# Optimization experiments

Hardware: AMD Instinct MI355X
Metric: run time of the kernel (lower is better)

## Reference

```python
import jax, jax.numpy as jnp
import numpy as np

B, N, D, H = 2, 1024, 1024, 16
DH = D // H
SCALE = 1.0 / DH ** 0.5
STJ_Q = 1.0
NUM_ITER = 4
CAUSAL = True
EPS = 1e-6


def setup_inputs() -> dict:
    key = jax.random.key(0)
    k1, k2, k3 = jax.random.split(key, 3)
    x = jax.random.normal(k1, (B, N, D), jnp.float32)
    Wqkv = jax.random.normal(k2, (3 * D, D), jnp.float32) / np.float32(np.sqrt(D))
    Wo = jax.random.normal(k3, (D, D), jnp.float32) / np.float32(np.sqrt(D))
    return {"x": x, "Wqkv": Wqkv, "Wo": Wo}


def stieltjes_attention(Q, K, V, scale, causal, q, num_iter):
    # Q,K,V: [B,H,N,dh]. Scores s: [B,H,N,N].
    n = Q.shape[2]
    s = jnp.einsum('bhnd,bhmd->bhnm', Q, K) * scale
    if causal:
        mask = jnp.tril(jnp.ones((n, n), bool))  # [N,N], True = attend
    else:
        mask = jnp.ones((n, n), bool)
    # Solve per-row lambda s.t. sum_j (lambda - s_j)^(-q) = 1 (Stieltjes-transform
    # normalization) with Newton iterations; masked entries contribute 0.
    s_masked = jnp.where(mask, s, -1e30)
    lam = s_masked.max(-1) + 1.0  # [B,H,N], start above max score
    for _ in range(num_iter):
        d = jnp.maximum(lam[..., None] - s, EPS)  # [B,H,N,N]
        w = jnp.where(mask, d ** (-q), 0.0)
        f = w.sum(-1) - 1.0
        fp = -q * jnp.where(mask, d ** (-q - 1.0), 0.0).sum(-1)
        lam = lam - f / fp
    d = jnp.maximum(lam[..., None] - s, EPS)
    p = jnp.where(mask, d ** (-q), 0.0)
    p = p / p.sum(-1, keepdims=True)  # final exact normalization
    return jnp.einsum('bhnm,bhmd->bhnd', p, V)


def reference(x, Wqkv, Wo):
    b, n, dmodel = x.shape
    qkv = (x @ Wqkv.T).reshape(b, n, 3, H, DH).transpose(2, 0, 3, 1, 4)
    Q, K, V = qkv[0], qkv[1], qkv[2]
    o = stieltjes_attention(Q, K, V, SCALE, CAUSAL, STJ_Q, NUM_ITER)
    o = o.transpose(0, 2, 1, 3).reshape(b, n, dmodel)
    return o @ Wo.T
```

## Files before the change

kernel.cpp:

```cpp
#include <hip/hip_runtime.h>
#include <hip/hip_bf16.h>
#include <math.h>

#define HNUM 16
#define DH 64
#define NSEQ 1024
#define BATCH 2
#define DMODEL 1024
#define SCALE 0.125f
#define EPS 1e-6f
#define NUM_ITER 4
#define SPAD 1128

typedef float f32x4 __attribute__((ext_vector_type(4)));
typedef short bfrag __attribute__((ext_vector_type(8)));
typedef unsigned int u32x4 __attribute__((ext_vector_type(4)));

__device__ inline float bf2f_u(unsigned int u) {
    return __builtin_bit_cast(float, u << 16);
}
__device__ inline unsigned short f2bf_u(float f) {
    return __builtin_bit_cast(unsigned short, __float2bfloat16(f));
}

__device__ inline void gload16(const __hip_bfloat16* g, __hip_bfloat16* l) {
    __builtin_amdgcn_global_load_lds(
        (const __attribute__((address_space(1))) void*)g,
        (__attribute__((address_space(3))) void*)l, 16, 0, 0);
}

__global__ __launch_bounds__(256) void cast3(const float* __restrict__ s0, __hip_bfloat16* __restrict__ d0, int n0,
                                             const float* __restrict__ s1, __hip_bfloat16* __restrict__ d1, int n1,
                                             const float* __restrict__ s2, __hip_bfloat16* __restrict__ d2, int n2) {
    const int stride = gridDim.x * blockDim.x;
    const int tot = n0 + n1 + n2;
    for (int i = blockIdx.x * blockDim.x + threadIdx.x; i < tot; i += stride) {
        const float* s; __hip_bfloat16* d; int off;
        if (i < n0)            { s = s0; d = d0; off = i; }
        else if (i < n0 + n1)  { s = s1; d = d1; off = i - n0; }
        else                   { s = s2; d = d2; off = i - n0 - n1; }
        const float4 v = *reinterpret_cast<const float4*>(&s[(size_t)off * 4]);
        ushort4 o;
        o.x = f2bf_u(v.x); o.y = f2bf_u(v.y); o.z = f2bf_u(v.z); o.w = f2bf_u(v.w);
        *reinterpret_cast<ushort4*>(&d[(size_t)off * 4]) = o;
    }
}

template <bool OUT_BF16>
__global__ __launch_bounds__(256) void gemm_bt(const __hip_bfloat16* __restrict__ A,
                                               const __hip_bfloat16* __restrict__ B,
                                               void* __restrict__ Cv,
                                               int M, int Nc, int K) {
    __shared__ __align__(16) __hip_bfloat16 As[128 * 64];
    __shared__ __align__(16) __hip_bfloat16 Bs[128 * 64];
    const int tid  = threadIdx.x;
    const int l    = tid & 63;
    const int wave = tid >> 6;
    const int m0 = blockIdx.y * 128, n0 = blockIdx.x * 128;
    const int wr = (wave >> 1) * 64, wc = (wave & 1) * 64;
    const int lr = l & 15;
    const int lk = (l >> 4) * 8;

    f32x4 acc[4][4];
#pragma unroll
    for (int m = 0; m < 4; ++m)
#pragma unroll
        for (int n = 0; n < 4; ++n) acc[m][n] = (f32x4){0.f, 0.f, 0.f, 0.f};

    for (int k0 = 0; k0 < K; k0 += 64) {
#pragma unroll
        for (int p = 0; p < 4; ++p) {
            const int idx = tid + p * 256;
            const int r = idx >> 3, ce = (idx & 7) * 8;
            gload16(&A[(size_t)(m0 + r) * K + k0 + ce], &As[idx * 8]);
        }
#pragma unroll
        for (int p = 0; p < 4; ++p) {
            const int idx = tid + p * 256;
            const int r = idx >> 3, ce = (idx & 7) * 8;
            gload16(&B[(size_t)(n0 + r) * K + k0 + ce], &Bs[idx * 8]);
        }
        __syncthreads();

#pragma unroll
        for (int kk = 0; kk < 64; kk += 32) {
            bfrag af[4], bfr[4];
#pragma unroll
            for (int m = 0; m < 4; ++m)
                af[m] = *reinterpret_cast<const bfrag*>(&As[(wr + m * 16 + lr) * 64 + kk + lk]);
#pragma unroll
            for (int n = 0; n < 4; ++n)
                bfr[n] = *reinterpret_cast<const bfrag*>(&Bs[(wc + n * 16 + lr) * 64 + kk + lk]);
#pragma unroll
            for (int m = 0; m < 4; ++m)
#pragma unroll
                for (int n = 0; n < 4; ++n)
                    acc[m][n] = __builtin_amdgcn_mfma_f32_16x16x32_bf16(
                        af[m], bfr[n], acc[m][n], 0, 0, 0);
        }
        __syncthreads();
    }

#pragma unroll
    for (int m = 0; m < 4; ++m) {
        const int row0 = m0 + wr + m * 16 + (l >> 4) * 4;
#pragma unroll
        for (int n = 0; n < 4; ++n) {
            const int col = n0 + wc + n * 16 + lr;
#pragma unroll
            for (int j = 0; j < 4; ++j) {
                if constexpr (OUT_BF16) {
                    ((__hip_bfloat16*)Cv)[(size_t)(row0 + j) * Nc + col] =
                        __float2bfloat16(acc[m][n][j]);
                } else {
                    ((float*)Cv)[(size_t)(row0 + j) * Nc + col] = acc[m][n][j];
                }
            }
        }
    }
}

__global__ __launch_bounds__(256) void transpose_v(const __hip_bfloat16* __restrict__ qkvb,
                                                   __hip_bfloat16* __restrict__ Vt) {
    const int bh = blockIdx.x >> 4;
    const int nc = blockIdx.x & 15;
    const int b = bh >> 4, h = bh & 15;
    __shared__ unsigned short tile[64][80];
    const int t = threadIdx.x;
    {
        const int r = t >> 2, cc = (t & 3) * 16;
        const size_t src = ((size_t)(b * NSEQ + nc * 64 + r)) * 3072 + 2048 + h * 64 + cc;
        const uint4 v0 = *reinterpret_cast<const uint4*>(&qkvb[src]);
        const uint4 v1 = *reinterpret_cast<const uint4*>(&qkvb[src + 8]);
        *reinterpret_cast<uint4*>(&tile[r][cc])     = v0;
        *reinterpret_cast<uint4*>(&tile[r][cc + 8]) = v1;
    }
    __syncthreads();
    {
        const int d = t >> 2, n2 = (t & 3) * 16;
        unsigned int e[16];
#pragma unroll
        for (int k = 0; k < 16; ++k) e[k] = tile[n2 + k][d];
        uint4 o0, o1;
        o0.x = e[0]  | (e[1]  << 16); o0.y = e[2]  | (e[3]  << 16);
        o0.z = e[4]  | (e[5]  << 16); o0.w = e[6]  | (e[7]  << 16);
        o1.x = e[8]  | (e[9]  << 16); o1.y = e[10] | (e[11] << 16);
        o1.z = e[12] | (e[13] << 16); o1.w = e[14] | (e[15] << 16);
        const size_t dst = ((size_t)(bh * 64 + d)) * 1024 + nc * 64 + n2;
        *reinterpret_cast<uint4*>(&Vt[dst])     = o0;
        *reinterpret_cast<uint4*>(&Vt[dst + 8]) = o1;
    }
}

template <int NQ>
__device__ inline void newton_row_wb(unsigned short* __restrict__ Srow,
                                     int ncols, int limit, int lane) {
    constexpr int NC = NQ * 2;
    float sv[NC * 2];
#pragma unroll
    for (int t = 0; t < NC; ++t) {
        const int c = lane * 2 + t * 128;
        const unsigned int u = *reinterpret_cast<const unsigned int*>(&Srow[c]);
        float v0 = bf2f_u(u & 0xffffu);
        float v1 = bf2f_u(u >> 16);
        if (t >= NC - 2) {
            v0 = (c     < ncols) ? v0 : -1e30f;
            v1 = (c + 1 < ncols) ? v1 : -1e30f;
        }
        sv[2 * t] = v0; sv[2 * t + 1] = v1;
    }

    float mx = sv[0];
#pragma unroll
    for (int e = 1; e < 2 * NC; ++e) mx = fmaxf(mx, sv[e]);
#pragma unroll
    for (int off = 32; off; off >>= 1) mx = fmaxf(mx, __shfl_xor(mx, off));
    float lam = mx + 1.0f;

    for (int it = 0; it < NUM_ITER; ++it) {
        float f = 0.f, fp = 0.f;
#pragma unroll
        for (int e = 0; e < 2 * NC; ++e) {
            const float inv = __builtin_amdgcn_rcpf(fmaxf(lam - sv[e], EPS));
            f += inv; fp = fmaf(inv, inv, fp);
        }
#pragma unroll
        for (int off = 32; off; off >>= 1) {
            f  += __shfl_xor(f, off);
            fp += __shfl_xor(fp, off);
        }
        lam += (f - 1.0f) / fp;
    }

    float sw = 0.f;
#pragma unroll
    for (int e = 0; e < 2 * NC; ++e) {
        sv[e] = __builtin_amdgcn_rcpf(fmaxf(lam - sv[e], EPS));
        sw += sv[e];
    }
#pragma unroll
    for (int off = 32; off; off >>= 1) sw += __shfl_xor(sw, off);
    const float isw = __builtin_amdgcn_rcpf(sw);

#pragma unroll
    for (int t = 0; t < NC; ++t) {
        const int c = lane * 2 + t * 128;
        if (t * 128 < limit && c < limit) {
            const unsigned int pk = (unsigned)f2bf_u(sv[2 * t] * isw)
                                  | ((unsigned)f2bf_u(sv[2 * t + 1] * isw) << 16);
            *reinterpret_cast<unsigned int*>(&Srow[c]) = pk;
        }
    }
}

__global__ __launch_bounds__(512) void attn_mfma(const __hip_bfloat16* __restrict__ qkvb,
                                                 const __hip_bfloat16* __restrict__ Vt,
                                                 __hip_bfloat16* __restrict__ obf) {
    const int tid  = threadIdx.x;
    const int lane = tid & 63;
    const int wave = tid >> 6;
    const int qt = blockIdx.x & 63;
    const int bh = blockIdx.x >> 6;
    const int b = bh >> 4, h = bh & 15;
    const int r0 = qt * 16;

    __shared__ __align__(16) unsigned short S[16][SPAD];
    __shared__ __align__(16) unsigned short Qs[16][72];

    const size_t qbase = (size_t)(b * NSEQ) * 3072;
    const int lr  = lane & 15;
    const int lk8 = (lane >> 4) * 8;

    if (tid < 128) {
        const int r = tid >> 3, c = (tid & 7) * 8;
        const uint4 v = *reinterpret_cast<const uint4*>(
            &qkvb[qbase + (size_t)(r0 + r) * 3072 + h * 64 + c]);
        *reinterpret_cast<uint4*>(&Qs[r][c]) = v;
    }
    __syncthreads();

    const __hip_bfloat16* kglob = qkvb + qbase + 1024 + h * 64;
    const int ntask = qt + 1;
    const bfrag a0 = *reinterpret_cast<const bfrag*>(&Qs[lr][lk8]);
    const bfrag a1 = *reinterpret_cast<const bfrag*>(&Qs[lr][32 + lk8]);
    for (int jt = wave; jt < ntask; jt += 8) {
        const int jrow = jt * 16 + lr;
        const bfrag b0 = *reinterpret_cast<const bfrag*>(&kglob[(size_t)jrow * 3072 + lk8]);
        const bfrag b1 = *reinterpret_cast<const bfrag*>(&kglob[(size_t)jrow * 3072 + 32 + lk8]);
        f32x4 c = (f32x4){0.f, 0.f, 0.f, 0.f};
        c = __builtin_amdgcn_mfma_f32_16x16x32_bf16(a0, b0, c, 0, 0, 0);
        c = __builtin_amdgcn_mfma_f32_16x16x32_bf16(a1, b1, c, 0, 0, 0);
#pragma unroll
        for (int j = 0; j < 4; ++j) {
            const int row = (lane >> 4) * 4 + j;
            S[row][jt * 16 + lr] = f2bf_u(c[j] * SCALE);
        }
    }
    __syncthreads();

    if (tid < 192) {
        const int row = tid / 12;
        const int cu  = tid - row * 12;
        *reinterpret_cast<u32x4*>(&S[row][r0 + 16 + cu * 8]) = (u32x4){0u, 0u, 0u, 0u};
    }
    const int limit = r0 + 16;
    for (int rr = 0; rr < 2; ++rr) {
        const int row   = wave * 2 + rr;
        const int ncols = r0 + row + 1;
        const int nq    = (ncols + 255) >> 8;
        switch (nq) {
            case 1:  newton_row_wb<1>(S[row], ncols, limit, lane); break;
            case 2:  newton_row_wb<2>(S[row], ncols, limit, lane); break;
            case 3:  newton_row_wb<3>(S[row], ncols, limit, lane); break;
            default: newton_row_wb<4>(S[row], ncols, limit, lane); break;
        }
    }
    __syncthreads();

    if (wave < 4) {
        const int dt = wave;
        const __hip_bfloat16* vtrow = Vt + ((size_t)(bh * 64 + dt * 16 + lr)) * 1024;

        f32x4 acc0 = (f32x4){0.f, 0.f, 0.f, 0.f};
        f32x4 acc1 = (f32x4){0.f, 0.f, 0.f, 0.f};
        for (int j0 = 0; j0 <= r0; j0 += 64) {
            {
                const bfrag pa = *reinterpret_cast<const bfrag*>(&S[lr][j0 + lk8]);
                const bfrag pb = *reinterpret_cast<const bfrag*>(&vtrow[j0 + lk8]);
                acc0 = __builtin_amdgcn_mfma_f32_16x16x32_bf16(pa, pb, acc0, 0, 0, 0);
            }
            if (j0 + 32 <= r0) {
                const bfrag pa = *reinterpret_cast<const bfrag*>(&S[lr][j0 + 32 + lk8]);
                const bfrag pb = *reinterpret_cast<const bfrag*>(&vtrow[j0 + 32 + lk8]);
                acc1 = __builtin_amdgcn_mfma_f32_16x16x32_bf16(pa, pb, acc1, 0, 0, 0);
            }
        }

#pragma unroll
        for (int j = 0; j < 4; ++j) {
            const int row = (lane >> 4) * 4 + j;
            obf[(size_t)(b * NSEQ + r0 + row) * 1024 + h * 64 + dt * 16 + lr] =
                __float2bfloat16(acc0[j] + acc1[j]);
        }
    }
}

extern "C" void kernel_launch(void* const* d_in, const int* in_sizes, int n_in,
                              void* d_out, int out_size, void* d_ws, size_t ws_size,
                              hipStream_t stream) {
    const float* x    = (const float*)d_in[0];
    const float* Wqkv = (const float*)d_in[1];
    const float* Wo   = (const float*)d_in[2];
    float* out = (float*)d_out;

    const int M = BATCH * NSEQ;
    char* ws = (char*)d_ws;
    __hip_bfloat16* xbf  = (__hip_bfloat16*)ws; ws += (size_t)M * DMODEL * 2;
    __hip_bfloat16* wqbf = (__hip_bfloat16*)ws; ws += (size_t)3 * DMODEL * DMODEL * 2;
    __hip_bfloat16* wobf = (__hip_bfloat16*)ws; ws += (size_t)DMODEL * DMODEL * 2;
    __hip_bfloat16* qkvb = (__hip_bfloat16*)ws; ws += (size_t)M * 3 * DMODEL * 2;
    __hip_bfloat16* Vt   = (__hip_bfloat16*)ws; ws += (size_t)BATCH * HNUM * DH * NSEQ * 2;
    __hip_bfloat16* obf  = (__hip_bfloat16*)ws; ws += (size_t)M * DMODEL * 2;

    dim3 blk(256);
    cast3<<<2048, blk, 0, stream>>>(x, xbf, M * DMODEL / 4,
                                    Wqkv, wqbf, 3 * DMODEL * DMODEL / 4,
                                    Wo, wobf, DMODEL * DMODEL / 4);

    dim3 g1(3 * DMODEL / 128, M / 128);
    gemm_bt<true><<<g1, blk, 0, stream>>>(xbf, wqbf, qkvb, M, 3 * DMODEL, DMODEL);

    transpose_v<<<512, blk, 0, stream>>>(qkvb, Vt);

    attn_mfma<<<2048, dim3(512), 0, stream>>>(qkvb, Vt, obf);

    dim3 g2(DMODEL / 128, M / 128);
    gemm_bt<false><<<g2, blk, 0, stream>>>(obf, wobf, out, M, DMODEL, DMODEL);
}
```

Baseline: 125.2 us.

## Shrink GEMM M-tile, interleave two Newton rows per wave, load Q fragments directly

The GEMM tile shrinks from 128x128 to 64x128, which doubles the grid size so more workgroups are in flight on the many compute units, at the cost of less reuse of each B tile. The Newton solver now processes a wave's two rows together, so the two independent reductions and reciprocal chains can hide each other's latency. Q fragments are read straight from global memory instead of being staged in LDS, which removes the Qs buffer and one barrier. Zeroing of the padding tile is folded into the score loop, and the S row padding is reduced to cut LDS use.

```diff
diff --git a/kernel.cpp b/kernel.cpp
--- a/kernel.cpp
+++ b/kernel.cpp
@@ -10,7 +10,7 @@
 #define SCALE 0.125f
 #define EPS 1e-6f
 #define NUM_ITER 4
-#define SPAD 1128
+#define SPAD 1048
 
 typedef float f32x4 __attribute__((ext_vector_type(4)));
 typedef short bfrag __attribute__((ext_vector_type(8)));
@@ -51,25 +51,25 @@
                                                const __hip_bfloat16* __restrict__ B,
                                                void* __restrict__ Cv,
                                                int M, int Nc, int K) {
-    __shared__ __align__(16) __hip_bfloat16 As[128 * 64];
+    __shared__ __align__(16) __hip_bfloat16 As[64 * 64];
     __shared__ __align__(16) __hip_bfloat16 Bs[128 * 64];
     const int tid  = threadIdx.x;
     const int l    = tid & 63;
     const int wave = tid >> 6;
-    const int m0 = blockIdx.y * 128, n0 = blockIdx.x * 128;
-    const int wr = (wave >> 1) * 64, wc = (wave & 1) * 64;
+    const int m0 = blockIdx.y * 64, n0 = blockIdx.x * 128;
+    const int wr = (wave >> 1) * 32, wc = (wave & 1) * 64;
     const int lr = l & 15;
     const int lk = (l >> 4) * 8;
 
-    f32x4 acc[4][4];
-#pragma unroll
-    for (int m = 0; m < 4; ++m)
+    f32x4 acc[2][4];
+#pragma unroll
+    for (int m = 0; m < 2; ++m)
 #pragma unroll
         for (int n = 0; n < 4; ++n) acc[m][n] = (f32x4){0.f, 0.f, 0.f, 0.f};
 
     for (int k0 = 0; k0 < K; k0 += 64) {
 #pragma unroll
-        for (int p = 0; p < 4; ++p) {
+        for (int p = 0; p < 2; ++p) {
             const int idx = tid + p * 256;
             const int r = idx >> 3, ce = (idx & 7) * 8;
             gload16(&A[(size_t)(m0 + r) * K + k0 + ce], &As[idx * 8]);
@@ -84,15 +84,15 @@
 
 #pragma unroll
         for (int kk = 0; kk < 64; kk += 32) {
-            bfrag af[4], bfr[4];
-#pragma unroll
-            for (int m = 0; m < 4; ++m)
+            bfrag af[2], bfr[4];
+#pragma unroll
+            for (int m = 0; m < 2; ++m)
                 af[m] = *reinterpret_cast<const bfrag*>(&As[(wr + m * 16 + lr) * 64 + kk + lk]);
 #pragma unroll
             for (int n = 0; n < 4; ++n)
                 bfr[n] = *reinterpret_cast<const bfrag*>(&Bs[(wc + n * 16 + lr) * 64 + kk + lk]);
 #pragma unroll
-            for (int m = 0; m < 4; ++m)
+            for (int m = 0; m < 2; ++m)
 #pragma unroll
                 for (int n = 0; n < 4; ++n)
                     acc[m][n] = __builtin_amdgcn_mfma_f32_16x16x32_bf16(
@@ -102,7 +102,7 @@
     }
 
 #pragma unroll
-    for (int m = 0; m < 4; ++m) {
+    for (int m = 0; m < 2; ++m) {
         const int row0 = m0 + wr + m * 16 + (l >> 4) * 4;
 #pragma unroll
         for (int n = 0; n < 4; ++n) {
@@ -153,62 +153,80 @@
 }
 
 template <int NQ>
-__device__ inline void newton_row_wb(unsigned short* __restrict__ Srow,
-                                     int ncols, int limit, int lane) {
+__device__ inline void newton2_wb(unsigned short* __restrict__ SA,
+                                  unsigned short* __restrict__ SB,
+                                  int ncolsA, int ncolsB, int limit, int lane) {
     constexpr int NC = NQ * 2;
-    float sv[NC * 2];
+    float svA[NC * 2], svB[NC * 2];
 #pragma unroll
     for (int t = 0; t < NC; ++t) {
         const int c = lane * 2 + t * 128;
-        const unsigned int u = *reinterpret_cast<const unsigned int*>(&Srow[c]);
-        float v0 = bf2f_u(u & 0xffffu);
-        float v1 = bf2f_u(u >> 16);
+        const unsigned int uA = *reinterpret_cast<const unsigned int*>(&SA[c]);
+        const unsigned int uB = *reinterpret_cast<const unsigned int*>(&SB[c]);
+        float a0 = bf2f_u(uA & 0xffffu), a1 = bf2f_u(uA >> 16);
+        float b0 = bf2f_u(uB & 0xffffu), b1 = bf2f_u(uB >> 16);
         if (t >= NC - 2) {
-            v0 = (c     < ncols) ? v0 : -1e30f;
-            v1 = (c + 1 < ncols) ? v1 : -1e30f;
-        }
-        sv[2 * t] = v0; sv[2 * t + 1] = v1;
-    }
-
-    float mx = sv[0];
-#pragma unroll
-    for (int e = 1; e < 2 * NC; ++e) mx = fmaxf(mx, sv[e]);
-#pragma unroll
-    for (int off = 32; off; off >>= 1) mx = fmaxf(mx, __shfl_xor(mx, off));
-    float lam = mx + 1.0f;
+            a0 = (c     < ncolsA) ? a0 : -1e30f;
+            a1 = (c + 1 < ncolsA) ? a1 : -1e30f;
+            b0 = (c     < ncolsB) ? b0 : -1e30f;
+            b1 = (c + 1 < ncolsB) ? b1 : -1e30f;
+        }
+        svA[2 * t] = a0; svA[2 * t + 1] = a1;
+        svB[2 * t] = b0; svB[2 * t + 1] = b1;
+    }
+
+    float mA = svA[0], mB = svB[0];
+#pragma unroll
+    for (int e = 1; e < 2 * NC; ++e) { mA = fmaxf(mA, svA[e]); mB = fmaxf(mB, svB[e]); }
+#pragma unroll
+    for (int off = 32; off; off >>= 1) {
+        mA = fmaxf(mA, __shfl_xor(mA, off));
+        mB = fmaxf(mB, __shfl_xor(mB, off));
+    }
+    float lamA = mA + 1.0f, lamB = mB + 1.0f;
 
     for (int it = 0; it < NUM_ITER; ++it) {
-        float f = 0.f, fp = 0.f;
+        float fA = 0.f, fpA = 0.f, fB = 0.f, fpB = 0.f;
 #pragma unroll
         for (int e = 0; e < 2 * NC; ++e) {
-            const float inv = __builtin_amdgcn_rcpf(fmaxf(lam - sv[e], EPS));
-            f += inv; fp = fmaf(inv, inv, fp);
+            const float iA = __builtin_amdgcn_rcpf(fmaxf(lamA - svA[e], EPS));
+            fA += iA; fpA = fmaf(iA, iA, fpA);
+            const float iB = __builtin_amdgcn_rcpf(fmaxf(lamB - svB[e], EPS));
+            fB += iB; fpB = fmaf(iB, iB, fpB);
         }
 #pragma unroll
         for (int off = 32; off; off >>= 1) {
-            f  += __shfl_xor(f, off);
-            fp += __shfl_xor(fp, off);
-        }
-        lam += (f - 1.0f) / fp;
-    }
-
-    float sw = 0.f;
+            fA += __shfl_xor(fA, off); fpA += __shfl_xor(fpA, off);
+            fB += __shfl_xor(fB, off); fpB += __shfl_xor(fpB, off);
+        }
+        lamA += (fA - 1.0f) / fpA;
+        lamB += (fB - 1.0f) / fpB;
+    }
+
+    float swA = 0.f, swB = 0.f;
 #pragma unroll
     for (int e = 0; e < 2 * NC; ++e) {
-        sv[e] = __builtin_amdgcn_rcpf(fmaxf(lam - sv[e], EPS));
-        sw += sv[e];
-    }
-#pragma unroll
-    for (int off = 32; off; off >>= 1) sw += __shfl_xor(sw, off);
-    const float isw = __builtin_amdgcn_rcpf(sw);
+        svA[e] = __builtin_amdgcn_rcpf(fmaxf(lamA - svA[e], EPS)); swA += svA[e];
+        svB[e] = __builtin_amdgcn_rcpf(fmaxf(lamB - svB[e], EPS)); swB += svB[e];
+    }
+#pragma unroll
+    for (int off = 32; off; off >>= 1) {
+        swA += __shfl_xor(swA, off);
+        swB += __shfl_xor(swB, off);
+    }
+    const float iswA = __builtin_amdgcn_rcpf(swA);
+    const float iswB = __builtin_amdgcn_rcpf(swB);
 
 #pragma unroll
     for (int t = 0; t < NC; ++t) {
         const int c = lane * 2 + t * 128;
         if (t * 128 < limit && c < limit) {
-            const unsigned int pk = (unsigned)f2bf_u(sv[2 * t] * isw)
-                                  | ((unsigned)f2bf_u(sv[2 * t + 1] * isw) << 16);
-            *reinterpret_cast<unsigned int*>(&Srow[c]) = pk;
+            const unsigned int pA = (unsigned)f2bf_u(svA[2 * t] * iswA)
+                                  | ((unsigned)f2bf_u(svA[2 * t + 1] * iswA) << 16);
+            *reinterpret_cast<unsigned int*>(&SA[c]) = pA;
+            const unsigned int pB = (unsigned)f2bf_u(svB[2 * t] * iswB)
+                                  | ((unsigned)f2bf_u(svB[2 * t + 1] * iswB) << 16);
+            *reinterpret_cast<unsigned int*>(&SB[c]) = pB;
         }
     }
 }
@@ -225,54 +243,45 @@
     const int r0 = qt * 16;
 
     __shared__ __align__(16) unsigned short S[16][SPAD];
-    __shared__ __align__(16) unsigned short Qs[16][72];
 
     const size_t qbase = (size_t)(b * NSEQ) * 3072;
     const int lr  = lane & 15;
     const int lk8 = (lane >> 4) * 8;
-
-    if (tid < 128) {
-        const int r = tid >> 3, c = (tid & 7) * 8;
-        const uint4 v = *reinterpret_cast<const uint4*>(
-            &qkvb[qbase + (size_t)(r0 + r) * 3072 + h * 64 + c]);
-        *reinterpret_cast<uint4*>(&Qs[r][c]) = v;
+    const int rj0 = (lane >> 4) * 4;
+
+    const __hip_bfloat16* qrow = qkvb + qbase + (size_t)(r0 + lr) * 3072 + h * 64;
+    const bfrag a0 = *reinterpret_cast<const bfrag*>(&qrow[lk8]);
+    const bfrag a1 = *reinterpret_cast<const bfrag*>(&qrow[32 + lk8]);
+    const __hip_bfloat16* kglob = qkvb + qbase + 1024 + h * 64;
+    for (int jt = wave; jt <= qt + 1; jt += 8) {
+        if (jt <= qt) {
+            const int jrow = jt * 16 + lr;
+            const bfrag b0 = *reinterpret_cast<const bfrag*>(&kglob[(size_t)jrow * 3072 + lk8]);
+            const bfrag b1 = *reinterpret_cast<const bfrag*>(&kglob[(size_t)jrow * 3072 + 32 + lk8]);
+            f32x4 c = (f32x4){0.f, 0.f, 0.f, 0.f};
+            c = __builtin_amdgcn_mfma_f32_16x16x32_bf16(a0, b0, c, 0, 0, 0);
+            c = __builtin_amdgcn_mfma_f32_16x16x32_bf16(a1, b1, c, 0, 0, 0);
+#pragma unroll
+            for (int j = 0; j < 4; ++j)
+                S[rj0 + j][jt * 16 + lr] = f2bf_u(c[j] * SCALE);
+        } else {
+#pragma unroll
+            for (int j = 0; j < 4; ++j)
+                S[rj0 + j][jt * 16 + lr] = 0;
+        }
     }
     __syncthreads();
 
-    const __hip_bfloat16* kglob = qkvb + qbase + 1024 + h * 64;
-    const int ntask = qt + 1;
-    const bfrag a0 = *reinterpret_cast<const bfrag*>(&Qs[lr][lk8]);
-    const bfrag a1 = *reinterpret_cast<const bfrag*>(&Qs[lr][32 + lk8]);
-    for (int jt = wave; jt < ntask; jt += 8) {
-        const int jrow = jt * 16 + lr;
-        const bfrag b0 = *reinterpret_cast<const bfrag*>(&kglob[(size_t)jrow * 3072 + lk8]);
-        const bfrag b1 = *reinterpret_cast<const bfrag*>(&kglob[(size_t)jrow * 3072 + 32 + lk8]);
-        f32x4 c = (f32x4){0.f, 0.f, 0.f, 0.f};
-        c = __builtin_amdgcn_mfma_f32_16x16x32_bf16(a0, b0, c, 0, 0, 0);
-        c = __builtin_amdgcn_mfma_f32_16x16x32_bf16(a1, b1, c, 0, 0, 0);
-#pragma unroll
-        for (int j = 0; j < 4; ++j) {
-            const int row = (lane >> 4) * 4 + j;
-            S[row][jt * 16 + lr] = f2bf_u(c[j] * SCALE);
-        }
-    }
-    __syncthreads();
-
-    if (tid < 192) {
-        const int row = tid / 12;
-        const int cu  = tid - row * 12;
-        *reinterpret_cast<u32x4*>(&S[row][r0 + 16 + cu * 8]) = (u32x4){0u, 0u, 0u, 0u};
-    }
-    const int limit = r0 + 16;
-    for (int rr = 0; rr < 2; ++rr) {
-        const int row   = wave * 2 + rr;
-        const int ncols = r0 + row + 1;
-        const int nq    = (ncols + 255) >> 8;
+    {
+        const int rowA = wave * 2, rowB = rowA + 1;
+        const int ncolsA = r0 + rowA + 1, ncolsB = r0 + rowB + 1;
+        const int limit = r0 + 16;
+        const int nq = (ncolsB + 255) >> 8;
         switch (nq) {
-            case 1:  newton_row_wb<1>(S[row], ncols, limit, lane); break;
-            case 2:  newton_row_wb<2>(S[row], ncols, limit, lane); break;
-            case 3:  newton_row_wb<3>(S[row], ncols, limit, lane); break;
-            default: newton_row_wb<4>(S[row], ncols, limit, lane); break;
+            case 1:  newton2_wb<1>(S[rowA], S[rowB], ncolsA, ncolsB, limit, lane); break;
+            case 2:  newton2_wb<2>(S[rowA], S[rowB], ncolsA, ncolsB, limit, lane); break;
+            case 3:  newton2_wb<3>(S[rowA], S[rowB], ncolsA, ncolsB, limit, lane); break;
+            default: newton2_wb<4>(S[rowA], S[rowB], ncolsA, ncolsB, limit, lane); break;
         }
     }
     __syncthreads();
@@ -298,7 +307,7 @@
 
 #pragma unroll
         for (int j = 0; j < 4; ++j) {
-            const int row = (lane >> 4) * 4 + j;
+            const int row = rj0 + j;
             obf[(size_t)(b * NSEQ + r0 + row) * 1024 + h * 64 + dt * 16 + lr] =
                 __float2bfloat16(acc0[j] + acc1[j]);
         }
@@ -327,13 +336,13 @@
                                     Wqkv, wqbf, 3 * DMODEL * DMODEL / 4,
                                     Wo, wobf, DMODEL * DMODEL / 4);
 
-    dim3 g1(3 * DMODEL / 128, M / 128);
+    dim3 g1(3 * DMODEL / 128, M / 64);
     gemm_bt<true><<<g1, blk, 0, stream>>>(xbf, wqbf, qkvb, M, 3 * DMODEL, DMODEL);
 
     transpose_v<<<512, blk, 0, stream>>>(qkvb, Vt);
 
     attn_mfma<<<2048, dim3(512), 0, stream>>>(qkvb, Vt, obf);
 
-    dim3 g2(DMODEL / 128, M / 128);
+    dim3 g2(DMODEL / 128, M / 64);
     gemm_bt<false><<<g2, blk, 0, stream>>>(obf, wobf, out, M, DMODEL, DMODEL);
 }
```

After: 122.1 us. 1.03x faster.
